# Performance work log

Measured on AMD Instinct MI355X. Metric: run time of the kernel, lower is better.

Reference implementation:

```python
import jax, jax.numpy as jnp
import numpy as np

NUM_HEADS = 8


def setup_inputs() -> dict:
    key = jax.random.key(0)
    ks = jax.random.split(key, 7)
    R, C, E = 16, 2048, 256
    x = jax.random.normal(ks[0], (R, C, E), dtype=jnp.float32)
    s = 0.02
    Wq = jax.random.normal(ks[1], (E, E), dtype=jnp.float32) * s
    bq = jax.random.normal(ks[2], (E,), dtype=jnp.float32) * s
    Wk = jax.random.normal(ks[3], (E, E), dtype=jnp.float32) * s
    bk = jax.random.normal(ks[4], (E,), dtype=jnp.float32) * s
    Wv = jax.random.normal(ks[5], (E, E), dtype=jnp.float32) * s
    bv = jax.random.normal(ks[6], (E,), dtype=jnp.float32) * s
    return {"x": x, "Wq": Wq, "bq": bq, "Wk": Wk, "bk": bk, "Wv": Wv, "bv": bv}


def _to_heads(y, R, C, H, hd):
    # [R,C,E] -> [R,C,H,hd] -> [R,H,C,hd] -> permute(2,1,0,3)=[C,H,R,hd] -> reshape [1,H,C,R*hd]
    y = y.reshape(R, C, H, hd).transpose(0, 2, 1, 3)
    y = jnp.transpose(y, (2, 1, 0, 3)).reshape(1, H, C, R * hd)
    return y


def reference(x, Wq, bq, Wk, bk, Wv, bv):
    R, C, E = x.shape
    H = NUM_HEADS
    hd = E // H
    q = _to_heads(x @ Wq.T + bq, R, C, H, hd)  # [1,H,C,d], d=R*hd
    k = _to_heads(x @ Wk.T + bk, R, C, H, hd)
    v = _to_heads(x @ Wv.T + bv, R, C, H, hd)
    d = q.shape[-1]
    q = jax.nn.softmax(q, axis=-1)
    k = jax.nn.softmax(k, axis=-2)  # softmax over the sequence (n) axis
    q = q * jnp.asarray(float(d) ** 0.5, dtype=q.dtype)  # note: +0.5 power, as in source pred()
    attn_weights = jnp.einsum('bhnd,bhmd->bhnm', q, k).sum(0)  # [H,C,C]
    context = jnp.einsum('bhnd,bhne->bhde', k, v)               # [1,H,d,d]
    out = jnp.einsum('bhnd,bhde->hbne', q, context)             # [H,1,C,d]
    out = out.reshape(H, C, R, hd)                              # faithful .view
    out = jnp.transpose(out, (2, 1, 0, 3)).reshape(R, C, E)
    return (out, attn_weights)
```

## Files before the change

kernel.cpp:

```cpp
#include <hip/hip_runtime.h>

typedef unsigned short u16;
typedef short bf16x8 __attribute__((ext_vector_type(8)));
typedef float f32x4 __attribute__((ext_vector_type(4)));

__device__ __forceinline__ u16 f2bf(float f) {
  union { float f; unsigned u; } v; v.f = f;
  unsigned r = v.u + 0x7fffu + ((v.u >> 16) & 1u);
  return (u16)(r >> 16);
}

#define MFMA_B16(a, b, c) __builtin_amdgcn_mfma_f32_16x16x32_bf16((a), (b), (c), 0, 0, 0)

template<int CHUNKS>
__device__ __forceinline__ void stage_tile(const u16* __restrict__ gbase, int ldg,
                                           u16* lds, int tid) {
  const int wave = tid >> 6, lane = tid & 63;
  const int r8 = lane >> 3, slot = lane & 7;
#pragma unroll
  for (int j = 0; j < CHUNKS / 4; ++j) {
    const int chunk = wave + j * 4;
    const int row = chunk * 8 + r8;
    const u16* g = gbase + (size_t)row * ldg + (((slot ^ (row & 7)) << 3));
    __builtin_amdgcn_global_load_lds(
        (const __attribute__((address_space(1))) void*)g,
        (__attribute__((address_space(3))) void*)(lds + chunk * 512),
        16, 0, 0);
  }
}

__global__ void __launch_bounds__(256) convert_kernel(
    const float* __restrict__ x, const float* __restrict__ Wq,
    const float* __restrict__ Wk, const float* __restrict__ Wv,
    u16* __restrict__ xb, u16* __restrict__ Wb) {
  int i = blockIdx.x * 256 + threadIdx.x;
  const int NX4 = 2097152;
  if (i < NX4) {
    const float4 v = ((const float4*)x)[i];
    ushort4 o; o.x = f2bf(v.x); o.y = f2bf(v.y); o.z = f2bf(v.z); o.w = f2bf(v.w);
    ((ushort4*)xb)[i] = o;
  } else {
    int j4 = i - NX4;
    int j = j4 * 4;
    const float* W = (j < 65536) ? Wq : ((j < 131072) ? Wk : Wv);
    const float4 v = *(const float4*)(W + (j & 65535));
    ushort4 o; o.x = f2bf(v.x); o.y = f2bf(v.y); o.z = f2bf(v.z); o.w = f2bf(v.w);
    ((ushort4*)Wb)[j4] = o;
  }
}

__global__ void __launch_bounds__(256) linear_kernel(
    const u16* __restrict__ xb, const u16* __restrict__ Wb,
    const float* __restrict__ bq, const float* __restrict__ bk, const float* __restrict__ bv,
    float* __restrict__ q_lin, float* __restrict__ k_lin, u16* __restrict__ vT) {
  __shared__ __align__(16) u16 As[128 * 64];
  __shared__ __align__(16) u16 Bs[64 * 64];
  const int tid = threadIdx.x;
  const int m0 = blockIdx.x * 128, n0 = blockIdx.y * 64;
  const int wave = tid >> 6, lane = tid & 63;
  const int wm = wave >> 1, wn = wave & 1;
  const int lrow = lane & 15, lk = lane >> 4;
  const f32x4 fzero = {0.f, 0.f, 0.f, 0.f};
  f32x4 acc[4][2];
  for (int a = 0; a < 4; ++a) for (int b = 0; b < 2; ++b) acc[a][b] = fzero;

  for (int k0 = 0; k0 < 256; k0 += 64) {
    __syncthreads();
    stage_tile<16>(xb + (size_t)m0 * 256 + k0, 256, As, tid);
    stage_tile<8>(Wb + (size_t)n0 * 256 + k0, 256, Bs, tid);
    __syncthreads();
    for (int ks = 0; ks < 2; ++ks) {
      bf16x8 a[4], b[2];
      for (int f = 0; f < 4; ++f) {
        int r = wm * 64 + f * 16 + lrow;
        a[f] = *(const bf16x8*)(As + r * 64 + (((ks * 4 + lk) ^ (r & 7)) * 8));
      }
      for (int f = 0; f < 2; ++f) {
        int r = wn * 32 + f * 16 + lrow;
        b[f] = *(const bf16x8*)(Bs + r * 64 + (((ks * 4 + lk) ^ (r & 7)) * 8));
      }
      for (int fm = 0; fm < 4; ++fm)
        for (int fn = 0; fn < 2; ++fn)
          acc[fm][fn] = MFMA_B16(a[fm], b[fn], acc[fm][fn]);
    }
  }
  for (int fm = 0; fm < 4; ++fm)
    for (int fn = 0; fn < 2; ++fn)
      for (int r = 0; r < 4; ++r) {
        int grow = wm * 64 + fm * 16 + lk * 4 + r;
        int gcol = wn * 32 + fn * 16 + lrow;
        int m = m0 + grow, j = n0 + gcol;
        int rx = m >> 11, c = m & 2047;
        int w = j >> 8, jj = j & 255, h = jj >> 5, e = jj & 31;
        int h2 = c >> 8, c2 = ((c & 255) << 3) + h, d2 = (rx << 5) + e;
        float bias = (w == 0) ? bq[jj] : ((w == 1) ? bk[jj] : bv[jj]);
        float val = acc[fm][fn][r] + bias;
        size_t qk_off = ((size_t)((h2 << 11) + c2) << 9) + d2;
        if (w == 0)      q_lin[qk_off] = val;
        else if (w == 1) k_lin[qk_off] = val;
        else             vT[(((size_t)(h2 << 9) + d2) << 11) + c2] = f2bf(val);
      }
}

__global__ void __launch_bounds__(256) softmax_q_kernel(
    const float* __restrict__ q_lin, u16* __restrict__ qb) {
  const int row = blockIdx.x, tid = threadIdx.x;
  const int wave = tid >> 6, lane = tid & 63;
  const float* src = q_lin + ((size_t)row << 9);
  float v0 = src[tid], v1 = src[tid + 256];
  float m = fmaxf(v0, v1);
  for (int o = 32; o; o >>= 1) m = fmaxf(m, __shfl_xor(m, o));
  __shared__ float red[8];
  if (lane == 0) red[wave] = m;
  __syncthreads();
  m = fmaxf(fmaxf(red[0], red[1]), fmaxf(red[2], red[3]));
  float e0 = expf(v0 - m), e1 = expf(v1 - m);
  float s = e0 + e1;
  for (int o = 32; o; o >>= 1) s += __shfl_xor(s, o);
  if (lane == 0) red[4 + wave] = s;
  __syncthreads();
  s = red[4] + red[5] + red[6] + red[7];
  float sc = 22.627416997969522f / s;
  u16* dst = qb + ((size_t)row << 9);
  dst[tid] = f2bf(e0 * sc);
  dst[tid + 256] = f2bf(e1 * sc);
}

__global__ void __launch_bounds__(256) softmax_k_part_kernel(
    const float* __restrict__ k_lin, float2* __restrict__ partials) {
  const int tid = threadIdx.x;
  const int dl = tid & 63, ng = tid >> 6;
  const int dt = blockIdx.x, h = blockIdx.y, nch = blockIdx.z;
  const int d = dt * 64 + dl;
  const float* base = k_lin + ((size_t)h << 20) + ((size_t)(nch * 128 + ng * 32) << 9) + d;
  float v[32];
  #pragma unroll
  for (int i = 0; i < 32; ++i) v[i] = base[(size_t)i << 9];
  float m = v[0];
  #pragma unroll
  for (int i = 1; i < 32; ++i) m = fmaxf(m, v[i]);
  __shared__ float2 red[4][64];
  red[ng][dl].x = m;
  __syncthreads();
  float M = fmaxf(fmaxf(red[0][dl].x, red[1][dl].x), fmaxf(red[2][dl].x, red[3][dl].x));
  float s = 0.f;
  #pragma unroll
  for (int i = 0; i < 32; ++i) s += __expf(v[i] - M);
  red[ng][dl].y = s;
  __syncthreads();
  if (ng == 0) {
    float S = red[0][dl].y + red[1][dl].y + red[2][dl].y + red[3][dl].y;
    partials[(((h * 8 + dt) * 16 + nch) << 6) + dl] = make_float2(M, S);
  }
}

__global__ void __launch_bounds__(256) softmax_k_norm_kernel(
    const float* __restrict__ k_lin, const float2* __restrict__ partials,
    u16* __restrict__ kb, u16* __restrict__ kT) {
  __shared__ __align__(16) u16 Ts[64 * 128];
  const int tid = threadIdx.x;
  const int dl = tid & 63, ng = tid >> 6;
  const int dt = blockIdx.x, h = blockIdx.y, nch = blockIdx.z;
  const int d0 = dt * 64, n0 = nch * 128;
  const float2* pb = partials + (((h * 8 + dt) * 16) << 6) + dl;
  float2 pj[16];
  float M = -3.0e38f;
  #pragma unroll
  for (int j = 0; j < 16; ++j) { pj[j] = pb[j << 6]; M = fmaxf(M, pj[j].x); }
  float S = 0.f;
  #pragma unroll
  for (int j = 0; j < 16; ++j) S += pj[j].y * __expf(pj[j].x - M);
  float inv = 1.0f / S;
  const float* src = k_lin + ((size_t)h << 20) + ((size_t)(n0 + ng * 32) << 9) + d0 + dl;
  u16* kbp = kb + ((size_t)h << 20) + ((size_t)(n0 + ng * 32) << 9) + d0 + dl;
  bf16x8 pk[4];
  #pragma unroll
  for (int i = 0; i < 32; ++i) {
    float e = __expf(src[(size_t)i << 9] - M) * inv;
    u16 b = f2bf(e);
    kbp[(size_t)i << 9] = b;
    pk[i >> 3][i & 7] = (short)b;
  }
  #pragma unroll
  for (int j = 0; j < 4; ++j) {
    int nl8 = ng * 4 + j;
    *(bf16x8*)(Ts + dl * 128 + (((nl8 * 8) ^ ((dl & 7) << 3)))) = pk[j];
  }
  __syncthreads();
  const int rd = tid >> 2;
  u16* kTp = kT + ((size_t)h << 20) + ((size_t)(d0 + rd) << 11) + n0;
  #pragma unroll
  for (int j = 0; j < 4; ++j) {
    int g = (tid & 3) + j * 4;
    bf16x8 vv = *(const bf16x8*)(Ts + rd * 128 + (((g * 8) ^ ((rd & 7) << 3))));
    *(bf16x8*)(kTp + g * 8) = vv;
  }
}

__global__ void __launch_bounds__(256) attn_kernel(
    const u16* __restrict__ qb, const u16* __restrict__ kb, float* __restrict__ attn) {
  __shared__ __align__(16) u16 As[128 * 64];
  __shared__ __align__(16) u16 Bs[128 * 64];
  const int tid = threadIdx.x, h = blockIdx.z;
  const int n0 = blockIdx.x * 128, mm0 = blockIdx.y * 128;
  const u16* A = qb + ((size_t)h << 20);
  const u16* B = kb + ((size_t)h << 20);
  const int wave = tid >> 6, lane = tid & 63;
  const int wm = wave >> 1, wn = wave & 1;
  const int lrow = lane & 15, lk = lane >> 4;
  const f32x4 fzero = {0.f, 0.f, 0.f, 0.f};
  f32x4 acc[4][4];
  for (int a = 0; a < 4; ++a) for (int b = 0; b < 4; ++b) acc[a][b] = fzero;

  for (int k0 = 0; k0 < 512; k0 += 64) {
    __syncthreads();
    stage_tile<16>(A + (size_t)n0 * 512 + k0, 512, As, tid);
    stage_tile<16>(B + (size_t)mm0 * 512 + k0, 512, Bs, tid);
    __syncthreads();
    for (int ks = 0; ks < 2; ++ks) {
      bf16x8 a[4], b[4];
      for (int f = 0; f < 4; ++f) {
        int r = wm * 64 + f * 16 + lrow;
        a[f] = *(const bf16x8*)(As + r * 64 + (((ks * 4 + lk) ^ (r & 7)) * 8));
      }
      for (int f = 0; f < 4; ++f) {
        int r = wn * 64 + f * 16 + lrow;
        b[f] = *(const bf16x8*)(Bs + r * 64 + (((ks * 4 + lk) ^ (r & 7)) * 8));
      }
      for (int fm = 0; fm < 4; ++fm)
        for (int fn = 0; fn < 4; ++fn)
          acc[fm][fn] = MFMA_B16(a[fm], b[fn], acc[fm][fn]);
    }
  }
  float* dst = attn + ((size_t)h << 22);
  for (int fm = 0; fm < 4; ++fm)
    for (int fn = 0; fn < 4; ++fn)
      for (int r = 0; r < 4; ++r) {
        int row = n0 + wm * 64 + fm * 16 + lk * 4 + r;
        int col = mm0 + wn * 64 + fn * 16 + lrow;
        dst[((size_t)row << 11) + col] = acc[fm][fn][r];
      }
}

__global__ void __launch_bounds__(256) ctx_kernel(
    const u16* __restrict__ vT, const u16* __restrict__ kT, u16* __restrict__ ctxT) {
  __shared__ __align__(16) u16 As[128 * 64];
  __shared__ __align__(16) u16 Bs[128 * 64];
  const int tid = threadIdx.x, h = blockIdx.z;
  const int e0 = blockIdx.x * 128, d0 = blockIdx.y * 128;
  const u16* A = vT + ((size_t)h << 20);
  const u16* B = kT + ((size_t)h << 20);
  const int wave = tid >> 6, lane = tid & 63;
  const int wm = wave >> 1, wn = wave & 1;
  const int lrow = lane & 15, lk = lane >> 4;
  const f32x4 fzero = {0.f, 0.f, 0.f, 0.f};
  f32x4 acc[4][4];
  for (int a = 0; a < 4; ++a) for (int b = 0; b < 4; ++b) acc[a][b] = fzero;

  for (int k0 = 0; k0 < 2048; k0 += 64) {
    __syncthreads();
    stage_tile<16>(A + (size_t)e0 * 2048 + k0, 2048, As, tid);
    stage_tile<16>(B + (size_t)d0 * 2048 + k0, 2048, Bs, tid);
    __syncthreads();
    for (int ks = 0; ks < 2; ++ks) {
      bf16x8 a[4], b[4];
      for (int f = 0; f < 4; ++f) {
        int r = wm * 64 + f * 16 + lrow;
        a[f] = *(const bf16x8*)(As + r * 64 + (((ks * 4 + lk) ^ (r & 7)) * 8));
      }
      for (int f = 0; f < 4; ++f) {
        int r = wn * 64 + f * 16 + lrow;
        b[f] = *(const bf16x8*)(Bs + r * 64 + (((ks * 4 + lk) ^ (r & 7)) * 8));
      }
      for (int fm = 0; fm < 4; ++fm)
        for (int fn = 0; fn < 4; ++fn)
          acc[fm][fn] = MFMA_B16(a[fm], b[fn], acc[fm][fn]);
    }
  }
  u16* dst = ctxT + ((size_t)h << 18);
  for (int fm = 0; fm < 4; ++fm)
    for (int fn = 0; fn < 4; ++fn)
      for (int r = 0; r < 4; ++r) {
        int erow = e0 + wm * 64 + fm * 16 + lk * 4 + r;
        int dcol = d0 + wn * 64 + fn * 16 + lrow;
        dst[((size_t)erow << 9) + dcol] = f2bf(acc[fm][fn][r]);
      }
}

__global__ void __launch_bounds__(256) out_kernel(
    const u16* __restrict__ qb, const u16* __restrict__ ctxT, float* __restrict__ out) {
  __shared__ __align__(16) u16 As[128 * 64];
  __shared__ __align__(16) u16 Bs[128 * 64];
  const int tid = threadIdx.x, h = blockIdx.z;
  const int n0 = blockIdx.x * 128, e0 = blockIdx.y * 128;
  const u16* A = qb + ((size_t)h << 20);
  const u16* B = ctxT + ((size_t)h << 18);
  const int wave = tid >> 6, lane = tid & 63;
  const int wm = wave >> 1, wn = wave & 1;
  const int lrow = lane & 15, lk = lane >> 4;
  const f32x4 fzero = {0.f, 0.f, 0.f, 0.f};
  f32x4 acc[4][4];
  for (int a = 0; a < 4; ++a) for (int b = 0; b < 4; ++b) acc[a][b] = fzero;

  for (int k0 = 0; k0 < 512; k0 += 64) {
    __syncthreads();
    stage_tile<16>(A + (size_t)n0 * 512 + k0, 512, As, tid);
    stage_tile<16>(B + (size_t)e0 * 512 + k0, 512, Bs, tid);
    __syncthreads();
    for (int ks = 0; ks < 2; ++ks) {
      bf16x8 a[4], b[4];
      for (int f = 0; f < 4; ++f) {
        int r = wm * 64 + f * 16 + lrow;
        a[f] = *(const bf16x8*)(As + r * 64 + (((ks * 4 + lk) ^ (r & 7)) * 8));
      }
      for (int f = 0; f < 4; ++f) {
        int r = wn * 64 + f * 16 + lrow;
        b[f] = *(const bf16x8*)(Bs + r * 64 + (((ks * 4 + lk) ^ (r & 7)) * 8));
      }
      for (int fm = 0; fm < 4; ++fm)
        for (int fn = 0; fn < 4; ++fn)
          acc[fm][fn] = MFMA_B16(a[fm], b[fn], acc[fm][fn]);
    }
  }
  for (int fm = 0; fm < 4; ++fm)
    for (int fn = 0; fn < 4; ++fn)
      for (int r = 0; r < 4; ++r) {
        int n = n0 + wm * 64 + fm * 16 + lk * 4 + r;
        int e = e0 + wn * 64 + fn * 16 + lrow;
        size_t dstIdx = ((size_t)(((e >> 5) << 11) + n) << 8) + (h << 5) + (e & 31);
        out[dstIdx] = acc[fm][fn][r];
      }
}

extern "C" void kernel_launch(void* const* d_in, const int* in_sizes, int n_in,
                              void* d_out, int out_size, void* d_ws, size_t ws_size,
                              hipStream_t stream) {
  const float* x  = (const float*)d_in[0];
  const float* Wq = (const float*)d_in[1];
  const float* bq = (const float*)d_in[2];
  const float* Wk = (const float*)d_in[3];
  const float* bk = (const float*)d_in[4];
  const float* Wv = (const float*)d_in[5];
  const float* bv = (const float*)d_in[6];
  float* out  = (float*)d_out;
  float* attn = out + 8388608;

  char* ws = (char*)d_ws;
  u16*   xb    = (u16*)(ws);
  u16*   Wb    = (u16*)(ws + 16777216);
  float* q_lin = (float*)(ws + 17170432);
  float* k_lin = (float*)(ws + 50724864);
  u16*   vT    = (u16*)(ws + 84279296);
  u16*   qb    = (u16*)(ws);
  u16*   kb    = (u16*)(ws + 17170432);
  u16*   kT    = (u16*)(ws + 33947648);
  u16*   ctxT  = (u16*)(ws + 50724864);
  float2* partials = (float2*)(attn + 33554432 - 131072);

  convert_kernel<<<8384, 256, 0, stream>>>(x, Wq, Wk, Wv, xb, Wb);
  linear_kernel<<<dim3(256, 12), 256, 0, stream>>>(xb, Wb, bq, bk, bv, q_lin, k_lin, vT);
  softmax_q_kernel<<<16384, 256, 0, stream>>>(q_lin, qb);
  softmax_k_part_kernel<<<dim3(8, 8, 16), 256, 0, stream>>>(k_lin, partials);
  softmax_k_norm_kernel<<<dim3(8, 8, 16), 256, 0, stream>>>(k_lin, partials, kb, kT);
  attn_kernel<<<dim3(16, 16, 8), 256, 0, stream>>>(qb, kb, attn);
  ctx_kernel<<<dim3(4, 4, 8), 256, 0, stream>>>(vT, kT, ctxT);
  out_kernel<<<dim3(16, 4, 8), 256, 0, stream>>>(qb, ctxT, out);
}
```

Before: 384.7 us.

## Use 256x256 tiles with 512 threads and split-K the context GEMM

All GEMM kernels move to a shared gemm_core with larger 256-row tiles, 8 waves per block and 8x4 MFMA fragments per wave, which raises data reuse per LDS load. The context GEMM, which previously had only 128 blocks each looping over K=2048, is split four ways along K into fp32 partials. A new reduce kernel sums the partials and converts them to bf16. This trades occupancy and register pressure for fewer blocks, more reuse and better parallelism in the ctx stage, and it adds an extra kernel plus a partial-buffer round trip.

```diff
diff --git a/kernel.cpp b/kernel.cpp
--- a/kernel.cpp
+++ b/kernel.cpp
@@ -12,20 +12,54 @@
 
 #define MFMA_B16(a, b, c) __builtin_amdgcn_mfma_f32_16x16x32_bf16((a), (b), (c), 0, 0, 0)
 
-template<int CHUNKS>
-__device__ __forceinline__ void stage_tile(const u16* __restrict__ gbase, int ldg,
-                                           u16* lds, int tid) {
+template<int ROWS>
+__device__ __forceinline__ void stage8(const u16* __restrict__ gbase, int ldg,
+                                       u16* lds, int tid) {
   const int wave = tid >> 6, lane = tid & 63;
   const int r8 = lane >> 3, slot = lane & 7;
 #pragma unroll
-  for (int j = 0; j < CHUNKS / 4; ++j) {
-    const int chunk = wave + j * 4;
+  for (int j = 0; j < ROWS / 64; ++j) {
+    const int chunk = wave + j * 8;
     const int row = chunk * 8 + r8;
-    const u16* g = gbase + (size_t)row * ldg + (((slot ^ (row & 7)) << 3));
+    const u16* g = gbase + (size_t)row * ldg + ((slot ^ (row & 7)) << 3);
     __builtin_amdgcn_global_load_lds(
         (const __attribute__((address_space(1))) void*)g,
         (__attribute__((address_space(3))) void*)(lds + chunk * 512),
         16, 0, 0);
+  }
+}
+
+template<int BN, int FN>
+__device__ __forceinline__ void gemm_core(const u16* __restrict__ A,
+                                          const u16* __restrict__ B,
+                                          int ldg, int kBeg, int kEnd,
+                                          u16* As, u16* Bs,
+                                          f32x4 (&acc)[8][FN], int tid) {
+  const int wave = tid >> 6, lane = tid & 63;
+  const int wm = wave >> 2, wn = wave & 3;
+  const int lrow = lane & 15, lk = lane >> 4;
+  for (int k0 = kBeg; k0 < kEnd; k0 += 64) {
+    __syncthreads();
+    stage8<256>(A + k0, ldg, As, tid);
+    stage8<BN>(B + k0, ldg, Bs, tid);
+    __syncthreads();
+#pragma unroll
+    for (int ks = 0; ks < 2; ++ks) {
+      bf16x8 b[FN];
+#pragma unroll
+      for (int fn = 0; fn < FN; ++fn) {
+        int r = wn * (BN / 4) + fn * 16 + lrow;
+        b[fn] = *(const bf16x8*)(Bs + r * 64 + (((ks * 4 + lk) ^ (r & 7)) * 8));
+      }
+#pragma unroll
+      for (int fm = 0; fm < 8; ++fm) {
+        int r = wm * 128 + fm * 16 + lrow;
+        bf16x8 a = *(const bf16x8*)(As + r * 64 + (((ks * 4 + lk) ^ (r & 7)) * 8));
+#pragma unroll
+        for (int fn = 0; fn < FN; ++fn)
+          acc[fm][fn] = MFMA_B16(a, b[fn], acc[fm][fn]);
+      }
+    }
   }
 }
 
@@ -49,49 +83,33 @@
   }
 }
 
-__global__ void __launch_bounds__(256) linear_kernel(
+__global__ void __launch_bounds__(512) linear_kernel(
     const u16* __restrict__ xb, const u16* __restrict__ Wb,
     const float* __restrict__ bq, const float* __restrict__ bk, const float* __restrict__ bv,
     float* __restrict__ q_lin, float* __restrict__ k_lin, u16* __restrict__ vT) {
-  __shared__ __align__(16) u16 As[128 * 64];
-  __shared__ __align__(16) u16 Bs[64 * 64];
+  __shared__ __align__(16) u16 As[256 * 64];
+  __shared__ __align__(16) u16 Bs[256 * 64];
   const int tid = threadIdx.x;
-  const int m0 = blockIdx.x * 128, n0 = blockIdx.y * 64;
-  const int wave = tid >> 6, lane = tid & 63;
-  const int wm = wave >> 1, wn = wave & 1;
+  const int m0 = blockIdx.x * 256, n0 = blockIdx.y * 256;
+  const int wave = tid >> 6, lane = tid & 63;
+  const int wm = wave >> 2, wn = wave & 3;
   const int lrow = lane & 15, lk = lane >> 4;
   const f32x4 fzero = {0.f, 0.f, 0.f, 0.f};
-  f32x4 acc[4][2];
-  for (int a = 0; a < 4; ++a) for (int b = 0; b < 2; ++b) acc[a][b] = fzero;
-
-  for (int k0 = 0; k0 < 256; k0 += 64) {
-    __syncthreads();
-    stage_tile<16>(xb + (size_t)m0 * 256 + k0, 256, As, tid);
-    stage_tile<8>(Wb + (size_t)n0 * 256 + k0, 256, Bs, tid);
-    __syncthreads();
-    for (int ks = 0; ks < 2; ++ks) {
-      bf16x8 a[4], b[2];
-      for (int f = 0; f < 4; ++f) {
-        int r = wm * 64 + f * 16 + lrow;
-        a[f] = *(const bf16x8*)(As + r * 64 + (((ks * 4 + lk) ^ (r & 7)) * 8));
-      }
-      for (int f = 0; f < 2; ++f) {
-        int r = wn * 32 + f * 16 + lrow;
-        b[f] = *(const bf16x8*)(Bs + r * 64 + (((ks * 4 + lk) ^ (r & 7)) * 8));
-      }
-      for (int fm = 0; fm < 4; ++fm)
-        for (int fn = 0; fn < 2; ++fn)
-          acc[fm][fn] = MFMA_B16(a[fm], b[fn], acc[fm][fn]);
-    }
-  }
-  for (int fm = 0; fm < 4; ++fm)
-    for (int fn = 0; fn < 2; ++fn)
+  f32x4 acc[8][4];
+  for (int a = 0; a < 8; ++a) for (int b = 0; b < 4; ++b) acc[a][b] = fzero;
+
+  gemm_core<256, 4>(xb + (size_t)m0 * 256, Wb + (size_t)n0 * 256, 256, 0, 256,
+                    As, Bs, acc, tid);
+
+  const int w = n0 >> 8;
+  for (int fm = 0; fm < 8; ++fm)
+    for (int fn = 0; fn < 4; ++fn)
       for (int r = 0; r < 4; ++r) {
-        int grow = wm * 64 + fm * 16 + lk * 4 + r;
-        int gcol = wn * 32 + fn * 16 + lrow;
+        int grow = wm * 128 + fm * 16 + lk * 4 + r;
+        int gcol = wn * 64 + fn * 16 + lrow;
         int m = m0 + grow, j = n0 + gcol;
         int rx = m >> 11, c = m & 2047;
-        int w = j >> 8, jj = j & 255, h = jj >> 5, e = jj & 31;
+        int jj = j & 255, h = jj >> 5, e = jj & 31;
         int h2 = c >> 8, c2 = ((c & 255) << 3) + h, d2 = (rx << 5) + e;
         float bias = (w == 0) ? bq[jj] : ((w == 1) ? bk[jj] : bv[jj]);
         float val = acc[fm][fn][r] + bias;
@@ -197,136 +215,96 @@
   }
 }
 
-__global__ void __launch_bounds__(256) attn_kernel(
+__global__ void __launch_bounds__(512) attn_kernel(
     const u16* __restrict__ qb, const u16* __restrict__ kb, float* __restrict__ attn) {
-  __shared__ __align__(16) u16 As[128 * 64];
+  __shared__ __align__(16) u16 As[256 * 64];
+  __shared__ __align__(16) u16 Bs[256 * 64];
+  const int tid = threadIdx.x, h = blockIdx.z;
+  const int n0 = blockIdx.x * 256, mm0 = blockIdx.y * 256;
+  const int wave = tid >> 6, lane = tid & 63;
+  const int wm = wave >> 2, wn = wave & 3;
+  const int lrow = lane & 15, lk = lane >> 4;
+  const f32x4 fzero = {0.f, 0.f, 0.f, 0.f};
+  f32x4 acc[8][4];
+  for (int a = 0; a < 8; ++a) for (int b = 0; b < 4; ++b) acc[a][b] = fzero;
+
+  gemm_core<256, 4>(qb + ((size_t)h << 20) + (size_t)n0 * 512,
+                    kb + ((size_t)h << 20) + (size_t)mm0 * 512,
+                    512, 0, 512, As, Bs, acc, tid);
+
+  float* dst = attn + ((size_t)h << 22);
+  for (int fm = 0; fm < 8; ++fm)
+    for (int fn = 0; fn < 4; ++fn)
+      for (int r = 0; r < 4; ++r) {
+        int row = n0 + wm * 128 + fm * 16 + lk * 4 + r;
+        int col = mm0 + wn * 64 + fn * 16 + lrow;
+        dst[((size_t)row << 11) + col] = acc[fm][fn][r];
+      }
+}
+
+__global__ void __launch_bounds__(512) ctx_kernel(
+    const u16* __restrict__ vT, const u16* __restrict__ kT, float* __restrict__ part) {
+  __shared__ __align__(16) u16 As[256 * 64];
+  __shared__ __align__(16) u16 Bs[256 * 64];
+  const int tid = threadIdx.x;
+  const int h = blockIdx.z >> 2, s = blockIdx.z & 3;
+  const int e0 = blockIdx.x * 256, d0 = blockIdx.y * 256;
+  const int wave = tid >> 6, lane = tid & 63;
+  const int wm = wave >> 2, wn = wave & 3;
+  const int lrow = lane & 15, lk = lane >> 4;
+  const f32x4 fzero = {0.f, 0.f, 0.f, 0.f};
+  f32x4 acc[8][4];
+  for (int a = 0; a < 8; ++a) for (int b = 0; b < 4; ++b) acc[a][b] = fzero;
+
+  gemm_core<256, 4>(vT + ((size_t)h << 20) + (size_t)e0 * 2048,
+                    kT + ((size_t)h << 20) + (size_t)d0 * 2048,
+                    2048, s * 512, s * 512 + 512, As, Bs, acc, tid);
+
+  float* dst = part + ((size_t)(s * 8 + h) << 18);
+  for (int fm = 0; fm < 8; ++fm)
+    for (int fn = 0; fn < 4; ++fn)
+      for (int r = 0; r < 4; ++r) {
+        int erow = e0 + wm * 128 + fm * 16 + lk * 4 + r;
+        int dcol = d0 + wn * 64 + fn * 16 + lrow;
+        dst[((size_t)erow << 9) + dcol] = acc[fm][fn][r];
+      }
+}
+
+__global__ void __launch_bounds__(256) ctx_reduce_kernel(
+    const float* __restrict__ part, u16* __restrict__ ctxT) {
+  int i = blockIdx.x * 256 + threadIdx.x;
+  const float4* p = (const float4*)part;
+  float4 s0 = p[i], s1 = p[i + (1 << 19)], s2 = p[i + (2 << 19)], s3 = p[i + 3 * (1 << 19)];
+  ushort4 o;
+  o.x = f2bf(s0.x + s1.x + s2.x + s3.x);
+  o.y = f2bf(s0.y + s1.y + s2.y + s3.y);
+  o.z = f2bf(s0.z + s1.z + s2.z + s3.z);
+  o.w = f2bf(s0.w + s1.w + s2.w + s3.w);
+  ((ushort4*)ctxT)[i] = o;
+}
+
+__global__ void __launch_bounds__(512) out_kernel(
+    const u16* __restrict__ qb, const u16* __restrict__ ctxT, float* __restrict__ out) {
+  __shared__ __align__(16) u16 As[256 * 64];
   __shared__ __align__(16) u16 Bs[128 * 64];
   const int tid = threadIdx.x, h = blockIdx.z;
-  const int n0 = blockIdx.x * 128, mm0 = blockIdx.y * 128;
-  const u16* A = qb + ((size_t)h << 20);
-  const u16* B = kb + ((size_t)h << 20);
-  const int wave = tid >> 6, lane = tid & 63;
-  const int wm = wave >> 1, wn = wave & 1;
+  const int n0 = blockIdx.x * 256, e0 = blockIdx.y * 128;
+  const int wave = tid >> 6, lane = tid & 63;
+  const int wm = wave >> 2, wn = wave & 3;
   const int lrow = lane & 15, lk = lane >> 4;
   const f32x4 fzero = {0.f, 0.f, 0.f, 0.f};
-  f32x4 acc[4][4];
-  for (int a = 0; a < 4; ++a) for (int b = 0; b < 4; ++b) acc[a][b] = fzero;
-
-  for (int k0 = 0; k0 < 512; k0 += 64) {
-    __syncthreads();
-    stage_tile<16>(A + (size_t)n0 * 512 + k0, 512, As, tid);
-    stage_tile<16>(B + (size_t)mm0 * 512 + k0, 512, Bs, tid);
-    __syncthreads();
-    for (int ks = 0; ks < 2; ++ks) {
-      bf16x8 a[4], b[4];
-      for (int f = 0; f < 4; ++f) {
-        int r = wm * 64 + f * 16 + lrow;
-        a[f] = *(const bf16x8*)(As + r * 64 + (((ks * 4 + lk) ^ (r & 7)) * 8));
-      }
-      for (int f = 0; f < 4; ++f) {
-        int r = wn * 64 + f * 16 + lrow;
-        b[f] = *(const bf16x8*)(Bs + r * 64 + (((ks * 4 + lk) ^ (r & 7)) * 8));
-      }
-      for (int fm = 0; fm < 4; ++fm)
-        for (int fn = 0; fn < 4; ++fn)
-          acc[fm][fn] = MFMA_B16(a[fm], b[fn], acc[fm][fn]);
-    }
-  }
-  float* dst = attn + ((size_t)h << 22);
-  for (int fm = 0; fm < 4; ++fm)
-    for (int fn = 0; fn < 4; ++fn)
+  f32x4 acc[8][2];
+  for (int a = 0; a < 8; ++a) for (int b = 0; b < 2; ++b) acc[a][b] = fzero;
+
+  gemm_core<128, 2>(qb + ((size_t)h << 20) + (size_t)n0 * 512,
+                    ctxT + ((size_t)h << 18) + (size_t)e0 * 512,
+                    512, 0, 512, As, Bs, acc, tid);
+
+  for (int fm = 0; fm < 8; ++fm)
+    for (int fn = 0; fn < 2; ++fn)
       for (int r = 0; r < 4; ++r) {
-        int row = n0 + wm * 64 + fm * 16 + lk * 4 + r;
-        int col = mm0 + wn * 64 + fn * 16 + lrow;
-        dst[((size_t)row << 11) + col] = acc[fm][fn][r];
-      }
-}
-
-__global__ void __launch_bounds__(256) ctx_kernel(
-    const u16* __restrict__ vT, const u16* __restrict__ kT, u16* __restrict__ ctxT) {
-  __shared__ __align__(16) u16 As[128 * 64];
-  __shared__ __align__(16) u16 Bs[128 * 64];
-  const int tid = threadIdx.x, h = blockIdx.z;
-  const int e0 = blockIdx.x * 128, d0 = blockIdx.y * 128;
-  const u16* A = vT + ((size_t)h << 20);
-  const u16* B = kT + ((size_t)h << 20);
-  const int wave = tid >> 6, lane = tid & 63;
-  const int wm = wave >> 1, wn = wave & 1;
-  const int lrow = lane & 15, lk = lane >> 4;
-  const f32x4 fzero = {0.f, 0.f, 0.f, 0.f};
-  f32x4 acc[4][4];
-  for (int a = 0; a < 4; ++a) for (int b = 0; b < 4; ++b) acc[a][b] = fzero;
-
-  for (int k0 = 0; k0 < 2048; k0 += 64) {
-    __syncthreads();
-    stage_tile<16>(A + (size_t)e0 * 2048 + k0, 2048, As, tid);
-    stage_tile<16>(B + (size_t)d0 * 2048 + k0, 2048, Bs, tid);
-    __syncthreads();
-    for (int ks = 0; ks < 2; ++ks) {
-      bf16x8 a[4], b[4];
-      for (int f = 0; f < 4; ++f) {
-        int r = wm * 64 + f * 16 + lrow;
-        a[f] = *(const bf16x8*)(As + r * 64 + (((ks * 4 + lk) ^ (r & 7)) * 8));
-      }
-      for (int f = 0; f < 4; ++f) {
-        int r = wn * 64 + f * 16 + lrow;
-        b[f] = *(const bf16x8*)(Bs + r * 64 + (((ks * 4 + lk) ^ (r & 7)) * 8));
-      }
-      for (int fm = 0; fm < 4; ++fm)
-        for (int fn = 0; fn < 4; ++fn)
-          acc[fm][fn] = MFMA_B16(a[fm], b[fn], acc[fm][fn]);
-    }
-  }
-  u16* dst = ctxT + ((size_t)h << 18);
-  for (int fm = 0; fm < 4; ++fm)
-    for (int fn = 0; fn < 4; ++fn)
-      for (int r = 0; r < 4; ++r) {
-        int erow = e0 + wm * 64 + fm * 16 + lk * 4 + r;
-        int dcol = d0 + wn * 64 + fn * 16 + lrow;
-        dst[((size_t)erow << 9) + dcol] = f2bf(acc[fm][fn][r]);
-      }
-}
-
-__global__ void __launch_bounds__(256) out_kernel(
-    const u16* __restrict__ qb, const u16* __restrict__ ctxT, float* __restrict__ out) {
-  __shared__ __align__(16) u16 As[128 * 64];
-  __shared__ __align__(16) u16 Bs[128 * 64];
-  const int tid = threadIdx.x, h = blockIdx.z;
-  const int n0 = blockIdx.x * 128, e0 = blockIdx.y * 128;
-  const u16* A = qb + ((size_t)h << 20);
-  const u16* B = ctxT + ((size_t)h << 18);
-  const int wave = tid >> 6, lane = tid & 63;
-  const int wm = wave >> 1, wn = wave & 1;
-  const int lrow = lane & 15, lk = lane >> 4;
-  const f32x4 fzero = {0.f, 0.f, 0.f, 0.f};
-  f32x4 acc[4][4];
-  for (int a = 0; a < 4; ++a) for (int b = 0; b < 4; ++b) acc[a][b] = fzero;
-
-  for (int k0 = 0; k0 < 512; k0 += 64) {
-    __syncthreads();
-    stage_tile<16>(A + (size_t)n0 * 512 + k0, 512, As, tid);
-    stage_tile<16>(B + (size_t)e0 * 512 + k0, 512, Bs, tid);
-    __syncthreads();
-    for (int ks = 0; ks < 2; ++ks) {
-      bf16x8 a[4], b[4];
-      for (int f = 0; f < 4; ++f) {
-        int r = wm * 64 + f * 16 + lrow;
-        a[f] = *(const bf16x8*)(As + r * 64 + (((ks * 4 + lk) ^ (r & 7)) * 8));
-      }
-      for (int f = 0; f < 4; ++f) {
-        int r = wn * 64 + f * 16 + lrow;
-        b[f] = *(const bf16x8*)(Bs + r * 64 + (((ks * 4 + lk) ^ (r & 7)) * 8));
-      }
-      for (int fm = 0; fm < 4; ++fm)
-        for (int fn = 0; fn < 4; ++fn)
-          acc[fm][fn] = MFMA_B16(a[fm], b[fn], acc[fm][fn]);
-    }
-  }
-  for (int fm = 0; fm < 4; ++fm)
-    for (int fn = 0; fn < 4; ++fn)
-      for (int r = 0; r < 4; ++r) {
-        int n = n0 + wm * 64 + fm * 16 + lk * 4 + r;
-        int e = e0 + wn * 64 + fn * 16 + lrow;
+        int n = n0 + wm * 128 + fm * 16 + lk * 4 + r;
+        int e = e0 + wn * 32 + fn * 16 + lrow;
         size_t dstIdx = ((size_t)(((e >> 5) << 11) + n) << 8) + (h << 5) + (e & 31);
         out[dstIdx] = acc[fm][fn][r];
       }
@@ -355,14 +333,16 @@
   u16*   kb    = (u16*)(ws + 17170432);
   u16*   kT    = (u16*)(ws + 33947648);
   u16*   ctxT  = (u16*)(ws + 50724864);
+  float* ctx_part = (float*)(ws + 134217728);
   float2* partials = (float2*)(attn + 33554432 - 131072);
 
   convert_kernel<<<8384, 256, 0, stream>>>(x, Wq, Wk, Wv, xb, Wb);
-  linear_kernel<<<dim3(256, 12), 256, 0, stream>>>(xb, Wb, bq, bk, bv, q_lin, k_lin, vT);
+  linear_kernel<<<dim3(128, 3), 512, 0, stream>>>(xb, Wb, bq, bk, bv, q_lin, k_lin, vT);
   softmax_q_kernel<<<16384, 256, 0, stream>>>(q_lin, qb);
   softmax_k_part_kernel<<<dim3(8, 8, 16), 256, 0, stream>>>(k_lin, partials);
   softmax_k_norm_kernel<<<dim3(8, 8, 16), 256, 0, stream>>>(k_lin, partials, kb, kT);
-  attn_kernel<<<dim3(16, 16, 8), 256, 0, stream>>>(qb, kb, attn);
-  ctx_kernel<<<dim3(4, 4, 8), 256, 0, stream>>>(vT, kT, ctxT);
-  out_kernel<<<dim3(16, 4, 8), 256, 0, stream>>>(qb, ctxT, out);
-}
+  attn_kernel<<<dim3(8, 8, 8), 512, 0, stream>>>(qb, kb, attn);
+  ctx_kernel<<<dim3(2, 2, 32), 512, 0, stream>>>(vT, kT, ctx_part);
+  ctx_reduce_kernel<<<2048, 256, 0, stream>>>(ctx_part, ctxT);
+  out_kernel<<<dim3(8, 4, 8), 512, 0, stream>>>(qb, ctxT, out);
+}
```

Measured after the change: 488.1 us. 1.27x slower.
